# Performance work log

Measured on AMD Instinct MI355X. Metric: run time of the kernel, lower is better.

## Reference

```python
import jax, jax.numpy as jnp
import numpy as np
from jax import lax


def _maxpool(x, kh, kw):
    # max_pool2d with stride 1 and 'same' padding (kh//2, kw//2)
    return lax.reduce_window(
        x, -jnp.inf, lax.max,
        window_dimensions=(1, 1, kh, kw),
        window_strides=(1, 1, 1, 1),
        padding=[(0, 0), (0, 0), (kh // 2, kh // 2), (kw // 2, kw // 2)])


def _minpool(x, kh, kw):
    # -max_pool2d(-x) == min pooling
    return lax.reduce_window(
        x, jnp.inf, lax.min,
        window_dimensions=(1, 1, kh, kw),
        window_strides=(1, 1, 1, 1),
        padding=[(0, 0), (0, 0), (kh // 2, kh // 2), (kw // 2, kw // 2)])


def soft_erode(img):
    p1 = _minpool(img, 3, 1)
    p2 = _minpool(img, 1, 3)
    return jnp.minimum(p1, p2)


def soft_dilate(img):
    return _maxpool(img, 3, 3)


def soft_open(img):
    return soft_dilate(soft_erode(img))


def setup_inputs() -> dict:
    key = jax.random.key(0)
    img = jax.random.uniform(key, (16, 1, 1024, 1024), dtype=jnp.float32)
    return {"img": img, "num_iter": 10}


def reference(img, num_iter):
    # soft skeleton via iterative thinning
    skel = jax.nn.relu(img - soft_open(img))
    img_eroded = img
    for _ in range(num_iter):  # fixed small trip count (static)
        img_eroded = soft_erode(img_eroded)
        delta = jax.nn.relu(img_eroded - soft_open(img_eroded))
        skel = skel + jax.nn.relu(delta - skel * delta)
    return skel
```

## Files before the change

kernel.cpp:

```cpp
#include <hip/hip_runtime.h>
#include <hip/hip_fp16.h>


#define W 1024
#define H 1024
#define NBATCH 16
#define RV 16

__device__ __forceinline__ uint32_t HMIN2(uint32_t a, uint32_t b) {
  uint32_t d;
  asm("v_pk_min_f16 %0, %1, %2" : "=v"(d) : "v"(a), "v"(b));
  return d;
}
__device__ __forceinline__ uint32_t HMAX2(uint32_t a, uint32_t b) {
  uint32_t d;
  asm("v_pk_max_f16 %0, %1, %2" : "=v"(d) : "v"(a), "v"(b));
  return d;
}
__device__ __forceinline__ uint32_t PKSUB(uint32_t a, uint32_t b) {
  uint32_t d;
  asm("v_pk_add_f16 %0, %1, %2 neg_lo:[0,1] neg_hi:[0,1]"
      : "=v"(d) : "v"(a), "v"(b));
  return d;
}
__device__ __forceinline__ uint32_t PKMUL(uint32_t a, uint32_t b) {
  uint32_t d;
  asm("v_pk_mul_f16 %0, %1, %2" : "=v"(d) : "v"(a), "v"(b));
  return d;
}
__device__ __forceinline__ uint32_t PKRELU(uint32_t a) {
  uint32_t d;
  asm("v_pk_max_f16 %0, %1, 0" : "=v"(d) : "v"(a));
  return d;
}
__device__ __forceinline__ uint32_t PK(float x, float y) {
  __half2 h = __floats2half2_rn(x, y);
  return *(uint32_t*)&h;
}
__device__ __forceinline__ float CVTLO(uint32_t u) {
  uint16_t t = (uint16_t)(u & 0xffffu);
  __half h = *(__half*)&t;
  return __half2float(h);
}
__device__ __forceinline__ float CVTHI(uint32_t u) {
  uint16_t t = (uint16_t)(u >> 16);
  __half h = *(__half*)&t;
  return __half2float(h);
}
__device__ __forceinline__ uint32_t SHUP(uint32_t x) {
  return (uint32_t)__builtin_amdgcn_update_dpp(0, (int)x, 0x138, 0xf, 0xf,
                                               true);
}
__device__ __forceinline__ uint32_t SHDN(uint32_t x) {
  return (uint32_t)__builtin_amdgcn_update_dpp(0, (int)x, 0x130, 0xf, 0xf,
                                               true);
}

#define STEP(P, C, N, DOH, DOU, K, INIT) {                                  \
  const uint32_t ca = F##C##a, cb = F##C##b;                                \
  const uint32_t na = F##N##a, nb = F##N##b;                                \
  const uint32_t vma = HMIN2(HMIN2(PMa, ca), na);                           \
  const uint32_t vmb = HMIN2(HMIN2(PMb, cb), nb);                           \
  const uint32_t t = SHUP(cb);                                              \
  const uint32_t r = SHDN(ca);                                              \
  const uint32_t m1 = mL ? (ca & 0xffffu) : (t >> 16);                      \
  const uint32_t r4 = mR ? (cb >> 16) : (r & 0xffffu);                      \
  const uint32_t sla = (ca >> 16) | (cb << 16);                             \
  const uint32_t slb = (cb >> 16) | (r4 << 16);                             \
  const uint32_t sra = m1 | (ca << 16);                                     \
  const uint32_t ea = HMIN2(vma, HMIN2(sra, sla));                          \
  const uint32_t eb = HMIN2(vmb, HMIN2(sla, slb));                          \
  if (DOH) {                                                                \
    const uint32_t te = SHUP(eb);                                           \
    const uint32_t re = SHDN(ea);                                           \
    const uint32_t em1 = mL ? (ea & 0xffffu) : (te >> 16);                  \
    const uint32_t er4 = mR ? (eb >> 16) : (re & 0xffffu);                  \
    const uint32_t esla = (ea >> 16) | (eb << 16);                          \
    const uint32_t eslb = (eb >> 16) | (er4 << 16);                         \
    const uint32_t esra = em1 | (ea << 16);                                 \
    const uint32_t hca = HMAX2(ea, HMAX2(esra, esla));                      \
    const uint32_t hcb = HMAX2(eb, HMAX2(esla, eslb));                      \
    if (DOU) {                                                              \
      uint32_t haa = h2a, hab = h2b, hba = hca, hbb = hcb;                  \
      if (K == 0 && top) { haa = h1a; hab = h1b; }                          \
      if (K == RV - 1 && bot) { hba = h1a; hbb = h1b; }                     \
      const uint32_t dda = HMAX2(HMAX2(haa, h1a), hba);                     \
      const uint32_t ddb = HMAX2(HMAX2(hab, h1b), hbb);                     \
      const uint32_t fa = PKSUB(ONE2, PKRELU(PKSUB(PMa, dda)));             \
      const uint32_t fb = PKSUB(ONE2, PKRELU(PKSUB(PMb, ddb)));             \
      if (INIT) { Q##K##a = fa; Q##K##b = fb; }                             \
      else { Q##K##a = PKMUL(Q##K##a, fa); Q##K##b = PKMUL(Q##K##b, fb); }  \
    }                                                                       \
    h2a = h1a; h2b = h1b; h1a = hca; h1b = hcb;                             \
  }                                                                         \
  F##P##a = ea; F##P##b = eb;                                               \
  PMa = ca; PMb = cb;                                                       \
}

#define STAGE_BEGIN uint32_t PMa = F0a, PMb = F0b,                          \
    h1a = 0, h1b = 0, h2a = 0, h2b = 0;

#define S_V30(INIT) { STAGE_BEGIN                                           \
  STEP(0,1,2,0,0,0,INIT)   STEP(1,2,3,0,0,0,INIT)   STEP(2,3,4,0,0,0,INIT)  \
  STEP(3,4,5,0,0,0,INIT)   STEP(4,5,6,0,0,0,INIT)                           \
  STEP(5,6,7,1,0,0,INIT)   STEP(6,7,8,1,0,0,INIT)                           \
  STEP(7,8,9,1,1,0,INIT)   STEP(8,9,10,1,1,1,INIT)                          \
  STEP(9,10,11,1,1,2,INIT) STEP(10,11,12,1,1,3,INIT)                        \
  STEP(11,12,13,1,1,4,INIT) STEP(12,13,14,1,1,5,INIT)                       \
  STEP(13,14,15,1,1,6,INIT) STEP(14,15,16,1,1,7,INIT)                       \
  STEP(15,16,17,1,1,8,INIT) STEP(16,17,18,1,1,9,INIT)                       \
  STEP(17,18,19,1,1,10,INIT) STEP(18,19,20,1,1,11,INIT)                     \
  STEP(19,20,21,1,1,12,INIT) STEP(20,21,22,1,1,13,INIT)                     \
  STEP(21,22,23,1,1,14,INIT) STEP(22,23,24,1,1,15,INIT)                     \
  STEP(23,24,25,0,0,0,INIT) STEP(24,25,26,0,0,0,INIT)                       \
  STEP(25,26,27,0,0,0,INIT) STEP(26,27,28,0,0,0,INIT)                       \
  STEP(27,28,29,0,0,0,INIT) }

#define S_V28 { STAGE_BEGIN                                                 \
  STEP(0,1,2,0,0,0,0)   STEP(1,2,3,0,0,0,0)   STEP(2,3,4,0,0,0,0)           \
  STEP(3,4,5,0,0,0,0)                                                       \
  STEP(4,5,6,1,0,0,0)   STEP(5,6,7,1,0,0,0)                                 \
  STEP(6,7,8,1,1,0,0)   STEP(7,8,9,1,1,1,0)   STEP(8,9,10,1,1,2,0)          \
  STEP(9,10,11,1,1,3,0) STEP(10,11,12,1,1,4,0) STEP(11,12,13,1,1,5,0)       \
  STEP(12,13,14,1,1,6,0) STEP(13,14,15,1,1,7,0) STEP(14,15,16,1,1,8,0)      \
  STEP(15,16,17,1,1,9,0) STEP(16,17,18,1,1,10,0) STEP(17,18,19,1,1,11,0)    \
  STEP(18,19,20,1,1,12,0) STEP(19,20,21,1,1,13,0) STEP(20,21,22,1,1,14,0)   \
  STEP(21,22,23,1,1,15,0)                                                   \
  STEP(22,23,24,0,0,0,0) STEP(23,24,25,0,0,0,0) STEP(24,25,26,0,0,0,0)      \
  STEP(25,26,27,0,0,0,0) }

#define S_V26 { STAGE_BEGIN                                                 \
  STEP(0,1,2,0,0,0,0)   STEP(1,2,3,0,0,0,0)   STEP(2,3,4,0,0,0,0)           \
  STEP(3,4,5,1,0,0,0)   STEP(4,5,6,1,0,0,0)                                 \
  STEP(5,6,7,1,1,0,0)   STEP(6,7,8,1,1,1,0)   STEP(7,8,9,1,1,2,0)           \
  STEP(8,9,10,1,1,3,0)  STEP(9,10,11,1,1,4,0) STEP(10,11,12,1,1,5,0)        \
  STEP(11,12,13,1,1,6,0) STEP(12,13,14,1,1,7,0) STEP(13,14,15,1,1,8,0)      \
  STEP(14,15,16,1,1,9,0) STEP(15,16,17,1,1,10,0) STEP(16,17,18,1,1,11,0)    \
  STEP(17,18,19,1,1,12,0) STEP(18,19,20,1,1,13,0) STEP(19,20,21,1,1,14,0)   \
  STEP(20,21,22,1,1,15,0)                                                   \
  STEP(21,22,23,0,0,0,0) STEP(22,23,24,0,0,0,0) STEP(23,24,25,0,0,0,0) }

#define S_V24 { STAGE_BEGIN                                                 \
  STEP(0,1,2,0,0,0,0)   STEP(1,2,3,0,0,0,0)                                 \
  STEP(2,3,4,1,0,0,0)   STEP(3,4,5,1,0,0,0)                                 \
  STEP(4,5,6,1,1,0,0)   STEP(5,6,7,1,1,1,0)   STEP(6,7,8,1,1,2,0)           \
  STEP(7,8,9,1,1,3,0)   STEP(8,9,10,1,1,4,0)  STEP(9,10,11,1,1,5,0)         \
  STEP(10,11,12,1,1,6,0) STEP(11,12,13,1,1,7,0) STEP(12,13,14,1,1,8,0)      \
  STEP(13,14,15,1,1,9,0) STEP(14,15,16,1,1,10,0) STEP(15,16,17,1,1,11,0)    \
  STEP(16,17,18,1,1,12,0) STEP(17,18,19,1,1,13,0) STEP(18,19,20,1,1,14,0)   \
  STEP(19,20,21,1,1,15,0)                                                   \
  STEP(20,21,22,0,0,0,0) STEP(21,22,23,0,0,0,0) }

#define S_V22 { STAGE_BEGIN                                                 \
  STEP(0,1,2,0,0,0,0)                                                       \
  STEP(1,2,3,1,0,0,0)   STEP(2,3,4,1,0,0,0)                                 \
  STEP(3,4,5,1,1,0,0)   STEP(4,5,6,1,1,1,0)   STEP(5,6,7,1,1,2,0)           \
  STEP(6,7,8,1,1,3,0)   STEP(7,8,9,1,1,4,0)   STEP(8,9,10,1,1,5,0)          \
  STEP(9,10,11,1,1,6,0) STEP(10,11,12,1,1,7,0) STEP(11,12,13,1,1,8,0)       \
  STEP(12,13,14,1,1,9,0) STEP(13,14,15,1,1,10,0) STEP(14,15,16,1,1,11,0)    \
  STEP(15,16,17,1,1,12,0) STEP(16,17,18,1,1,13,0) STEP(17,18,19,1,1,14,0)   \
  STEP(18,19,20,1,1,15,0)                                                   \
  STEP(19,20,21,0,0,0,0) }

#define S_V20 { STAGE_BEGIN                                                 \
  STEP(0,1,2,1,0,0,0)   STEP(1,2,3,1,0,0,0)                                 \
  STEP(2,3,4,1,1,0,0)   STEP(3,4,5,1,1,1,0)   STEP(4,5,6,1,1,2,0)           \
  STEP(5,6,7,1,1,3,0)   STEP(6,7,8,1,1,4,0)   STEP(7,8,9,1,1,5,0)           \
  STEP(8,9,10,1,1,6,0)  STEP(9,10,11,1,1,7,0) STEP(10,11,12,1,1,8,0)        \
  STEP(11,12,13,1,1,9,0) STEP(12,13,14,1,1,10,0) STEP(13,14,15,1,1,11,0)    \
  STEP(14,15,16,1,1,12,0) STEP(15,16,17,1,1,13,0) STEP(16,17,18,1,1,14,0)   \
  STEP(17,18,19,1,1,15,0) }

#define DECLF(i) uint32_t F##i##a, F##i##b;

#define COMMON_SETUP                                                        \
  const int l = threadIdx.x & 63;                                           \
  const int wid = threadIdx.x >> 6;                                         \
  const int w = blockIdx.x;                                                 \
  const int y0 = (blockIdx.y * 2 + wid) * RV;                               \
  const size_t base = (size_t)blockIdx.z * (size_t)(W * H);                 \
  const int rx = 208 * w - 8 + 4 * l;                                       \
  const int cq = min(max(rx, 0), W - 4);                                    \
  const bool mL = (rx == 0);                                                \
  const bool mR = (rx == W - 4);                                            \
  const bool top = (y0 == 0);                                               \
  const bool bot = (y0 + RV == H);                                          \
  const int wend = min(208 * (w + 1), W);                                   \
  const bool wr = (rx >= 208 * w) && (rx < wend);                           \
  const uint32_t ONE2 = 0x3C003C00u;

__global__ __launch_bounds__(128) void skel6(const float* __restrict__ in,
                                             uint16_t* __restrict__ e16,
                                             uint16_t* __restrict__ q16) {
  COMMON_SETUP
  DECLF(0) DECLF(1) DECLF(2) DECLF(3) DECLF(4) DECLF(5) DECLF(6) DECLF(7)
  DECLF(8) DECLF(9) DECLF(10) DECLF(11) DECLF(12) DECLF(13) DECLF(14)
  DECLF(15) DECLF(16) DECLF(17) DECLF(18) DECLF(19) DECLF(20) DECLF(21)
  DECLF(22) DECLF(23) DECLF(24) DECLF(25) DECLF(26) DECLF(27) DECLF(28)
  DECLF(29)
  uint32_t Q0a, Q0b, Q1a, Q1b, Q2a, Q2b, Q3a, Q3b;
  uint32_t Q4a, Q4b, Q5a, Q5b, Q6a, Q6b, Q7a, Q7b;
  uint32_t Q8a, Q8b, Q9a, Q9b, Q10a, Q10b, Q11a, Q11b;
  uint32_t Q12a, Q12b, Q13a, Q13b, Q14a, Q14b, Q15a, Q15b;

#define LOADROW1(i) {                                                       \
    const int gy = min(max(y0 - 7 + i, 0), H - 1);                          \
    const float4 v = *(const float4*)(in + base + (size_t)gy * W + cq);     \
    F##i##a = PK(v.x, v.y); F##i##b = PK(v.z, v.w); }
  LOADROW1(0) LOADROW1(1) LOADROW1(2) LOADROW1(3) LOADROW1(4) LOADROW1(5)
  LOADROW1(6) LOADROW1(7) LOADROW1(8) LOADROW1(9) LOADROW1(10) LOADROW1(11)
  LOADROW1(12) LOADROW1(13) LOADROW1(14) LOADROW1(15) LOADROW1(16)
  LOADROW1(17) LOADROW1(18) LOADROW1(19) LOADROW1(20) LOADROW1(21)
  LOADROW1(22) LOADROW1(23) LOADROW1(24) LOADROW1(25) LOADROW1(26)
  LOADROW1(27) LOADROW1(28) LOADROW1(29)
#undef LOADROW1

  S_V30(1) S_V28 S_V26 S_V24 S_V22 S_V20

  if (wr) {
#define STOREQ(k) {                                                         \
      *(uint2*)(q16 + base + (size_t)(y0 + k) * W + rx) =                   \
          make_uint2(Q##k##a, Q##k##b); }
    STOREQ(0) STOREQ(1) STOREQ(2) STOREQ(3)
    STOREQ(4) STOREQ(5) STOREQ(6) STOREQ(7)
    STOREQ(8) STOREQ(9) STOREQ(10) STOREQ(11)
    STOREQ(12) STOREQ(13) STOREQ(14) STOREQ(15)
#undef STOREQ
#define STOREE(k, j) {                                                      \
      *(uint2*)(e16 + base + (size_t)(y0 + k) * W + rx) =                   \
          make_uint2(F##j##a, F##j##b); }
    STOREE(0, 1) STOREE(1, 2) STOREE(2, 3) STOREE(3, 4)
    STOREE(4, 5) STOREE(5, 6) STOREE(6, 7) STOREE(7, 8)
    STOREE(8, 9) STOREE(9, 10) STOREE(10, 11) STOREE(11, 12)
    STOREE(12, 13) STOREE(13, 14) STOREE(14, 15) STOREE(15, 16)
#undef STOREE
  }
}

__global__ __launch_bounds__(128) void skel5(const uint16_t* __restrict__ e16,
                                             const uint16_t* __restrict__ q16,
                                             float* __restrict__ skel) {
  COMMON_SETUP
  DECLF(0) DECLF(1) DECLF(2) DECLF(3) DECLF(4) DECLF(5) DECLF(6) DECLF(7)
  DECLF(8) DECLF(9) DECLF(10) DECLF(11) DECLF(12) DECLF(13) DECLF(14)
  DECLF(15) DECLF(16) DECLF(17) DECLF(18) DECLF(19) DECLF(20) DECLF(21)
  DECLF(22) DECLF(23) DECLF(24) DECLF(25) DECLF(26) DECLF(27)
  uint32_t Q0a, Q0b, Q1a, Q1b, Q2a, Q2b, Q3a, Q3b;
  uint32_t Q4a, Q4b, Q5a, Q5b, Q6a, Q6b, Q7a, Q7b;
  uint32_t Q8a, Q8b, Q9a, Q9b, Q10a, Q10b, Q11a, Q11b;
  uint32_t Q12a, Q12b, Q13a, Q13b, Q14a, Q14b, Q15a, Q15b;

#define LOADROW2(i) {                                                       \
    const int gy = min(max(y0 - 6 + i, 0), H - 1);                          \
    const uint2 v = *(const uint2*)(e16 + base + (size_t)gy * W + cq);      \
    F##i##a = v.x; F##i##b = v.y; }
  LOADROW2(0) LOADROW2(1) LOADROW2(2) LOADROW2(3) LOADROW2(4) LOADROW2(5)
  LOADROW2(6) LOADROW2(7) LOADROW2(8) LOADROW2(9) LOADROW2(10) LOADROW2(11)
  LOADROW2(12) LOADROW2(13) LOADROW2(14) LOADROW2(15) LOADROW2(16)
  LOADROW2(17) LOADROW2(18) LOADROW2(19) LOADROW2(20) LOADROW2(21)
  LOADROW2(22) LOADROW2(23) LOADROW2(24) LOADROW2(25) LOADROW2(26)
  LOADROW2(27)
#undef LOADROW2

#define LOADQ(k) {                                                          \
    const uint2 v = *(const uint2*)(q16 + base + (size_t)(y0 + k) * W + cq); \
    Q##k##a = v.x; Q##k##b = v.y; }
  LOADQ(0) LOADQ(1) LOADQ(2) LOADQ(3) LOADQ(4) LOADQ(5) LOADQ(6) LOADQ(7)
  LOADQ(8) LOADQ(9) LOADQ(10) LOADQ(11) LOADQ(12) LOADQ(13) LOADQ(14)
  LOADQ(15)
#undef LOADQ

  S_V28 S_V26 S_V24 S_V22 S_V20

  if (wr) {
#define STOREQ(k) {                                                         \
      float4 s;                                                             \
      s.x = 1.0f - CVTLO(Q##k##a); s.y = 1.0f - CVTHI(Q##k##a);             \
      s.z = 1.0f - CVTLO(Q##k##b); s.w = 1.0f - CVTHI(Q##k##b);             \
      *(float4*)(skel + base + (size_t)(y0 + k) * W + rx) = s; }
    STOREQ(0) STOREQ(1) STOREQ(2) STOREQ(3)
    STOREQ(4) STOREQ(5) STOREQ(6) STOREQ(7)
    STOREQ(8) STOREQ(9) STOREQ(10) STOREQ(11)
    STOREQ(12) STOREQ(13) STOREQ(14) STOREQ(15)
#undef STOREQ
  }
}

extern "C" void kernel_launch(void* const* d_in, const int* in_sizes, int n_in,
                              void* d_out, int out_size, void* d_ws,
                              size_t ws_size, hipStream_t stream) {
  const float* img = (const float*)d_in[0];
  float* skel = (float*)d_out;
  const size_t NPIX = (size_t)NBATCH * W * H;
  uint16_t* E = (uint16_t*)d_ws;
  uint16_t* Q = E + NPIX;

  dim3 grid(5, H / (2 * RV), NBATCH);
  skel6<<<grid, 128, 0, stream>>>(img, E, Q);
  skel5<<<grid, 128, 0, stream>>>(E, Q, skel);
}
```

Measured before the change: 101.1 us.

## Narrow per-lane column tile from four to two pixels and double grid width

Each lane now holds two fp16 pixels per row (one packed register) instead of four, so a wave covers 128 columns with 112 useful outputs, and the grid doubles in x to 10 column tiles. This halves the register footprint per thread, which should raise occupancy and latency hiding. The cost is a larger fraction of redundant halo columns (16 of 128 instead of 16 of 256), more DPP shuffles per useful pixel, and narrower memory transactions.

After: 108.5 us. 1.07x slower.

```diff
diff --git a/kernel.cpp b/kernel.cpp
--- a/kernel.cpp
+++ b/kernel.cpp
@@ -57,48 +57,40 @@
 }
 
 #define STEP(P, C, N, DOH, DOU, K, INIT) {                                  \
-  const uint32_t ca = F##C##a, cb = F##C##b;                                \
-  const uint32_t na = F##N##a, nb = F##N##b;                                \
-  const uint32_t vma = HMIN2(HMIN2(PMa, ca), na);                           \
-  const uint32_t vmb = HMIN2(HMIN2(PMb, cb), nb);                           \
-  const uint32_t t = SHUP(cb);                                              \
-  const uint32_t r = SHDN(ca);                                              \
-  const uint32_t m1 = mL ? (ca & 0xffffu) : (t >> 16);                      \
-  const uint32_t r4 = mR ? (cb >> 16) : (r & 0xffffu);                      \
-  const uint32_t sla = (ca >> 16) | (cb << 16);                             \
-  const uint32_t slb = (cb >> 16) | (r4 << 16);                             \
-  const uint32_t sra = m1 | (ca << 16);                                     \
-  const uint32_t ea = HMIN2(vma, HMIN2(sra, sla));                          \
-  const uint32_t eb = HMIN2(vmb, HMIN2(sla, slb));                          \
+  const uint32_t c = F##C;                                                  \
+  const uint32_t n = F##N;                                                  \
+  const uint32_t vm = HMIN2(HMIN2(PM, c), n);                               \
+  const uint32_t t = SHUP(c);                                               \
+  const uint32_t r = SHDN(c);                                               \
+  const uint32_t lf = mL ? (c & 0xffffu) : (t >> 16);                       \
+  const uint32_t rt = mR ? (c >> 16) : (r & 0xffffu);                       \
+  const uint32_t sra = lf | (c << 16);                     \
+  const uint32_t sla = (c >> 16) | (rt << 16);            \
+  const uint32_t e = HMIN2(vm, HMIN2(sra, sla));                            \
   if (DOH) {                                                                \
-    const uint32_t te = SHUP(eb);                                           \
-    const uint32_t re = SHDN(ea);                                           \
-    const uint32_t em1 = mL ? (ea & 0xffffu) : (te >> 16);                  \
-    const uint32_t er4 = mR ? (eb >> 16) : (re & 0xffffu);                  \
-    const uint32_t esla = (ea >> 16) | (eb << 16);                          \
-    const uint32_t eslb = (eb >> 16) | (er4 << 16);                         \
-    const uint32_t esra = em1 | (ea << 16);                                 \
-    const uint32_t hca = HMAX2(ea, HMAX2(esra, esla));                      \
-    const uint32_t hcb = HMAX2(eb, HMAX2(esla, eslb));                      \
+    const uint32_t te = SHUP(e);                                            \
+    const uint32_t re = SHDN(e);                                            \
+    const uint32_t elf = mL ? (e & 0xffffu) : (te >> 16);                   \
+    const uint32_t ert = mR ? (e >> 16) : (re & 0xffffu);                   \
+    const uint32_t esra = elf | (e << 16);                                  \
+    const uint32_t esla = (e >> 16) | (ert << 16);                          \
+    const uint32_t hc = HMAX2(e, HMAX2(esra, esla));                        \
     if (DOU) {                                                              \
-      uint32_t haa = h2a, hab = h2b, hba = hca, hbb = hcb;                  \
-      if (K == 0 && top) { haa = h1a; hab = h1b; }                          \
-      if (K == RV - 1 && bot) { hba = h1a; hbb = h1b; }                     \
-      const uint32_t dda = HMAX2(HMAX2(haa, h1a), hba);                     \
-      const uint32_t ddb = HMAX2(HMAX2(hab, h1b), hbb);                     \
-      const uint32_t fa = PKSUB(ONE2, PKRELU(PKSUB(PMa, dda)));             \
-      const uint32_t fb = PKSUB(ONE2, PKRELU(PKSUB(PMb, ddb)));             \
-      if (INIT) { Q##K##a = fa; Q##K##b = fb; }                             \
-      else { Q##K##a = PKMUL(Q##K##a, fa); Q##K##b = PKMUL(Q##K##b, fb); }  \
+      uint32_t ha = h2, hb = hc;                                            \
+      if (K == 0 && top) { ha = h1; }                                       \
+      if (K == RV - 1 && bot) { hb = h1; }                                  \
+      const uint32_t dd = HMAX2(HMAX2(ha, h1), hb);                         \
+      const uint32_t f = PKSUB(ONE2, PKRELU(PKSUB(PM, dd)));                \
+      if (INIT) { Q##K = f; }                                               \
+      else { Q##K = PKMUL(Q##K, f); }                                       \
     }                                                                       \
-    h2a = h1a; h2b = h1b; h1a = hca; h1b = hcb;                             \
+    h2 = h1; h1 = hc;                                                       \
   }                                                                         \
-  F##P##a = ea; F##P##b = eb;                                               \
-  PMa = ca; PMb = cb;                                                       \
-}
-
-#define STAGE_BEGIN uint32_t PMa = F0a, PMb = F0b,                          \
-    h1a = 0, h1b = 0, h2a = 0, h2b = 0;
+  F##P = e;                                                                 \
+  PM = c;                                                                   \
+}
+
+#define STAGE_BEGIN uint32_t PM = F0, h1 = 0, h2 = 0;
 
 #define S_V30(INIT) { STAGE_BEGIN                                           \
   STEP(0,1,2,0,0,0,INIT)   STEP(1,2,3,0,0,0,INIT)   STEP(2,3,4,0,0,0,INIT)  \
@@ -171,7 +163,7 @@
   STEP(14,15,16,1,1,12,0) STEP(15,16,17,1,1,13,0) STEP(16,17,18,1,1,14,0)   \
   STEP(17,18,19,1,1,15,0) }
 
-#define DECLF(i) uint32_t F##i##a, F##i##b;
+#define DECLF(i) uint32_t F##i;
 
 #define COMMON_SETUP                                                        \
   const int l = threadIdx.x & 63;                                           \
@@ -179,14 +171,14 @@
   const int w = blockIdx.x;                                                 \
   const int y0 = (blockIdx.y * 2 + wid) * RV;                               \
   const size_t base = (size_t)blockIdx.z * (size_t)(W * H);                 \
-  const int rx = 208 * w - 8 + 4 * l;                                       \
-  const int cq = min(max(rx, 0), W - 4);                                    \
+  const int rx = 112 * w - 8 + 2 * l;                                       \
+  const int cq = min(max(rx, 0), W - 2);                                    \
   const bool mL = (rx == 0);                                                \
-  const bool mR = (rx == W - 4);                                            \
+  const bool mR = (rx == W - 2);                                            \
   const bool top = (y0 == 0);                                               \
   const bool bot = (y0 + RV == H);                                          \
-  const int wend = min(208 * (w + 1), W);                                   \
-  const bool wr = (rx >= 208 * w) && (rx < wend);                           \
+  const int wend = min(112 * (w + 1), W);                                   \
+  const bool wr = (rx >= 112 * w) && (rx < wend);                           \
   const uint32_t ONE2 = 0x3C003C00u;
 
 __global__ __launch_bounds__(128) void skel6(const float* __restrict__ in,
@@ -198,37 +190,32 @@
   DECLF(15) DECLF(16) DECLF(17) DECLF(18) DECLF(19) DECLF(20) DECLF(21)
   DECLF(22) DECLF(23) DECLF(24) DECLF(25) DECLF(26) DECLF(27) DECLF(28)
   DECLF(29)
-  uint32_t Q0a, Q0b, Q1a, Q1b, Q2a, Q2b, Q3a, Q3b;
-  uint32_t Q4a, Q4b, Q5a, Q5b, Q6a, Q6b, Q7a, Q7b;
-  uint32_t Q8a, Q8b, Q9a, Q9b, Q10a, Q10b, Q11a, Q11b;
-  uint32_t Q12a, Q12b, Q13a, Q13b, Q14a, Q14b, Q15a, Q15b;
-
-#define LOADROW1(i) {                                                       \
+  uint32_t Q0, Q1, Q2, Q3, Q4, Q5, Q6, Q7;
+  uint32_t Q8, Q9, Q10, Q11, Q12, Q13, Q14, Q15;
+
+#define LOADROW(i) {                                                        \
     const int gy = min(max(y0 - 7 + i, 0), H - 1);                          \
-    const float4 v = *(const float4*)(in + base + (size_t)gy * W + cq);     \
-    F##i##a = PK(v.x, v.y); F##i##b = PK(v.z, v.w); }
-  LOADROW1(0) LOADROW1(1) LOADROW1(2) LOADROW1(3) LOADROW1(4) LOADROW1(5)
-  LOADROW1(6) LOADROW1(7) LOADROW1(8) LOADROW1(9) LOADROW1(10) LOADROW1(11)
-  LOADROW1(12) LOADROW1(13) LOADROW1(14) LOADROW1(15) LOADROW1(16)
-  LOADROW1(17) LOADROW1(18) LOADROW1(19) LOADROW1(20) LOADROW1(21)
-  LOADROW1(22) LOADROW1(23) LOADROW1(24) LOADROW1(25) LOADROW1(26)
-  LOADROW1(27) LOADROW1(28) LOADROW1(29)
-#undef LOADROW1
+    const float2 v = *(const float2*)(in + base + (size_t)gy * W + cq);     \
+    F##i = PK(v.x, v.y); }
+  LOADROW(0) LOADROW(1) LOADROW(2) LOADROW(3) LOADROW(4) LOADROW(5)
+  LOADROW(6) LOADROW(7) LOADROW(8) LOADROW(9) LOADROW(10) LOADROW(11)
+  LOADROW(12) LOADROW(13) LOADROW(14) LOADROW(15) LOADROW(16) LOADROW(17)
+  LOADROW(18) LOADROW(19) LOADROW(20) LOADROW(21) LOADROW(22) LOADROW(23)
+  LOADROW(24) LOADROW(25) LOADROW(26) LOADROW(27) LOADROW(28) LOADROW(29)
+#undef LOADROW
 
   S_V30(1) S_V28 S_V26 S_V24 S_V22 S_V20
 
   if (wr) {
-#define STOREQ(k) {                                                         \
-      *(uint2*)(q16 + base + (size_t)(y0 + k) * W + rx) =                   \
-          make_uint2(Q##k##a, Q##k##b); }
+#define STOREQ(k)                                                           \
+    *(uint32_t*)(q16 + base + (size_t)(y0 + k) * W + rx) = Q##k;
     STOREQ(0) STOREQ(1) STOREQ(2) STOREQ(3)
     STOREQ(4) STOREQ(5) STOREQ(6) STOREQ(7)
     STOREQ(8) STOREQ(9) STOREQ(10) STOREQ(11)
     STOREQ(12) STOREQ(13) STOREQ(14) STOREQ(15)
 #undef STOREQ
-#define STOREE(k, j) {                                                      \
-      *(uint2*)(e16 + base + (size_t)(y0 + k) * W + rx) =                   \
-          make_uint2(F##j##a, F##j##b); }
+#define STOREE(k, j)                                                        \
+    *(uint32_t*)(e16 + base + (size_t)(y0 + k) * W + rx) = F##j;
     STOREE(0, 1) STOREE(1, 2) STOREE(2, 3) STOREE(3, 4)
     STOREE(4, 5) STOREE(5, 6) STOREE(6, 7) STOREE(7, 8)
     STOREE(8, 9) STOREE(9, 10) STOREE(10, 11) STOREE(11, 12)
@@ -245,26 +232,21 @@
   DECLF(8) DECLF(9) DECLF(10) DECLF(11) DECLF(12) DECLF(13) DECLF(14)
   DECLF(15) DECLF(16) DECLF(17) DECLF(18) DECLF(19) DECLF(20) DECLF(21)
   DECLF(22) DECLF(23) DECLF(24) DECLF(25) DECLF(26) DECLF(27)
-  uint32_t Q0a, Q0b, Q1a, Q1b, Q2a, Q2b, Q3a, Q3b;
-  uint32_t Q4a, Q4b, Q5a, Q5b, Q6a, Q6b, Q7a, Q7b;
-  uint32_t Q8a, Q8b, Q9a, Q9b, Q10a, Q10b, Q11a, Q11b;
-  uint32_t Q12a, Q12b, Q13a, Q13b, Q14a, Q14b, Q15a, Q15b;
-
-#define LOADROW2(i) {                                                       \
+  uint32_t Q0, Q1, Q2, Q3, Q4, Q5, Q6, Q7;
+  uint32_t Q8, Q9, Q10, Q11, Q12, Q13, Q14, Q15;
+
+#define LOADROW(i) {                                                        \
     const int gy = min(max(y0 - 6 + i, 0), H - 1);                          \
-    const uint2 v = *(const uint2*)(e16 + base + (size_t)gy * W + cq);      \
-    F##i##a = v.x; F##i##b = v.y; }
-  LOADROW2(0) LOADROW2(1) LOADROW2(2) LOADROW2(3) LOADROW2(4) LOADROW2(5)
-  LOADROW2(6) LOADROW2(7) LOADROW2(8) LOADROW2(9) LOADROW2(10) LOADROW2(11)
-  LOADROW2(12) LOADROW2(13) LOADROW2(14) LOADROW2(15) LOADROW2(16)
-  LOADROW2(17) LOADROW2(18) LOADROW2(19) LOADROW2(20) LOADROW2(21)
-  LOADROW2(22) LOADROW2(23) LOADROW2(24) LOADROW2(25) LOADROW2(26)
-  LOADROW2(27)
-#undef LOADROW2
-
-#define LOADQ(k) {                                                          \
-    const uint2 v = *(const uint2*)(q16 + base + (size_t)(y0 + k) * W + cq); \
-    Q##k##a = v.x; Q##k##b = v.y; }
+    F##i = *(const uint32_t*)(e16 + base + (size_t)gy * W + cq); }
+  LOADROW(0) LOADROW(1) LOADROW(2) LOADROW(3) LOADROW(4) LOADROW(5)
+  LOADROW(6) LOADROW(7) LOADROW(8) LOADROW(9) LOADROW(10) LOADROW(11)
+  LOADROW(12) LOADROW(13) LOADROW(14) LOADROW(15) LOADROW(16) LOADROW(17)
+  LOADROW(18) LOADROW(19) LOADROW(20) LOADROW(21) LOADROW(22) LOADROW(23)
+  LOADROW(24) LOADROW(25) LOADROW(26) LOADROW(27)
+#undef LOADROW
+
+#define LOADQ(k)                                                            \
+  Q##k = *(const uint32_t*)(q16 + base + (size_t)(y0 + k) * W + cq);
   LOADQ(0) LOADQ(1) LOADQ(2) LOADQ(3) LOADQ(4) LOADQ(5) LOADQ(6) LOADQ(7)
   LOADQ(8) LOADQ(9) LOADQ(10) LOADQ(11) LOADQ(12) LOADQ(13) LOADQ(14)
   LOADQ(15)
@@ -274,10 +256,10 @@
 
   if (wr) {
 #define STOREQ(k) {                                                         \
-      float4 s;                                                             \
-      s.x = 1.0f - CVTLO(Q##k##a); s.y = 1.0f - CVTHI(Q##k##a);             \
-      s.z = 1.0f - CVTLO(Q##k##b); s.w = 1.0f - CVTHI(Q##k##b);             \
-      *(float4*)(skel + base + (size_t)(y0 + k) * W + rx) = s; }
+      float2 s;                                                             \
+      s.x = 1.0f - CVTLO(Q##k);                                             \
+      s.y = 1.0f - CVTHI(Q##k);                                             \
+      *(float2*)(skel + base + (size_t)(y0 + k) * W + rx) = s; }
     STOREQ(0) STOREQ(1) STOREQ(2) STOREQ(3)
     STOREQ(4) STOREQ(5) STOREQ(6) STOREQ(7)
     STOREQ(8) STOREQ(9) STOREQ(10) STOREQ(11)
@@ -295,7 +277,7 @@
   uint16_t* E = (uint16_t*)d_ws;
   uint16_t* Q = E + NPIX;
 
-  dim3 grid(5, H / (2 * RV), NBATCH);
+  dim3 grid(10, H / (2 * RV), NBATCH);
   skel6<<<grid, 128, 0, stream>>>(img, E, Q);
   skel5<<<grid, 128, 0, stream>>>(E, Q, skel);
 }
```
